# Kernel tuning notes

Hardware: AMD Instinct MI355X
Metric: run time of the kernel (lower is better)

The kernel has to match this reference:

```python
import jax, jax.numpy as jnp
import numpy as np

TEMPERATURE = 0.1
EPS = 1e-12  # tf.math.l2_normalize epsilon

BATCH = 512
DIM = 256
QUEUE = 65536


def l2_normalize(x, axis=1):
    sq = jnp.sum(x * x, axis=axis, keepdims=True)
    return x * jax.lax.rsqrt(jnp.maximum(sq, EPS))


def setup_inputs() -> dict:
    key = jax.random.key(0)
    k1, k2, k3 = jax.random.split(key, 3)
    projections_1 = jax.random.normal(k1, (BATCH, DIM), dtype=jnp.float32)
    projections_2 = jax.random.normal(k2, (BATCH, DIM), dtype=jnp.float32)
    feature_queue = l2_normalize(jax.random.normal(k3, (QUEUE, DIM), dtype=jnp.float32), axis=1)
    return {"projections_1": projections_1, "projections_2": projections_2, "feature_queue": feature_queue}


def nearest_neighbour(projections, feature_queue):
    # [B, Q] similarity vs the memory queue, 1-NN retrieval + gather
    support_similarities = jnp.einsum('bd,qd->bq', projections, feature_queue)
    nn_idx = jnp.argmax(support_similarities, axis=1)
    nn_projections = feature_queue[nn_idx]  # [B, D]
    # straight-through: forward value is nn, gradient flows to projections
    return projections + jax.lax.stop_gradient(nn_projections - projections)


def reference(projections_1, projections_2, feature_queue):
    p1 = l2_normalize(projections_1, axis=1)
    p2 = l2_normalize(projections_2, axis=1)

    nn1 = nearest_neighbour(p1, feature_queue)
    nn2 = nearest_neighbour(p2, feature_queue)

    s_1_2_1 = jnp.einsum('bd,cd->bc', nn1, p2) / TEMPERATURE
    s_1_2_2 = jnp.einsum('bd,cd->bc', p2, nn1) / TEMPERATURE
    s_2_1_1 = jnp.einsum('bd,cd->bc', nn2, p1) / TEMPERATURE
    s_2_1_2 = jnp.einsum('bd,cd->bc', p1, nn2) / TEMPERATURE

    logits = jnp.concatenate([s_1_2_1, s_1_2_2, s_2_1_1, s_2_1_2], axis=0)  # [4B, B]
    batch = p1.shape[0]
    labels = jnp.tile(jnp.arange(batch), 4)  # [4B]

    # sparse categorical crossentropy from logits
    logp = jax.nn.log_softmax(logits, axis=-1)
    loss = -logp[jnp.arange(4 * batch), labels]  # [4B]

    # FIFO queue update (normalized projections_1 pushed in front)
    new_queue = jnp.concatenate([p1, feature_queue[:-batch]], axis=0)
    return loss, new_queue
```

## Files before the change

### kernel.cpp

```cpp
#include <hip/hip_runtime.h>
#include <stdint.h>


#define BATCH  512
#define DIM    256
#define QUEUE  65536
#define MROWS  1024
#define NGRP   2048
#define MARGIN 0.01f

typedef short bf16x8 __attribute__((ext_vector_type(8)));
typedef float f32x4  __attribute__((ext_vector_type(4)));

__device__ __forceinline__ unsigned int mono_f32(float f) {
    unsigned int u = __float_as_uint(f);
    return (u & 0x80000000u) ? ~u : (u | 0x80000000u);
}
__device__ __forceinline__ float unmono_f32(unsigned int m) {
    unsigned int u = (m & 0x80000000u) ? (m ^ 0x80000000u) : ~m;
    return __uint_as_float(u);
}
__device__ __forceinline__ unsigned short f2bf(float f) {
    unsigned int u = __float_as_uint(f);
    return (unsigned short)((u + 0x7fffu + ((u >> 16) & 1u)) >> 16);
}

__global__ __launch_bounds__(256)
void k01_prep(const float* __restrict__ queue, float* __restrict__ outq,
              char* __restrict__ Qbf,
              const float* __restrict__ p1, const float* __restrict__ p2,
              float* __restrict__ Pn, float* __restrict__ PnT,
              unsigned short* __restrict__ PhiF,
              unsigned int* __restrict__ rowmaxU, unsigned long long* __restrict__ rowfinal)
{
    const int bid = blockIdx.x;
    const int t = threadIdx.x;

    if (bid < 2048) {
        const int n0 = bid * 32;
        const f32x4* qsrc = (const f32x4*)(queue + (size_t)n0 * DIM);
        f32x4* qdst = (f32x4*)(outq + (size_t)(n0 + BATCH) * DIM);
        char* tile = Qbf + (size_t)(bid >> 1) * 32768;

        f32x4 va[8];
        #pragma unroll
        for (int it = 0; it < 4; ++it) {
            const int L = it * 256 + t;
            const int r = L >> 5, c16 = L & 31;
            va[2 * it]     = qsrc[(size_t)r * 64 + c16 * 2];
            va[2 * it + 1] = qsrc[(size_t)r * 64 + c16 * 2 + 1];
        }
        #pragma unroll
        for (int it = 0; it < 4; ++it) {
            const int L = it * 256 + t;
            const int r = L >> 5, c16 = L & 31;
            f32x4 v0 = va[2 * it], v1 = va[2 * it + 1];
            if (n0 + r < QUEUE - BATCH) {
                qdst[(size_t)r * 64 + c16 * 2]     = v0;
                qdst[(size_t)r * 64 + c16 * 2 + 1] = v1;
            }
            bf16x8 bb;
            bb[0] = (short)f2bf(v0.x); bb[1] = (short)f2bf(v0.y);
            bb[2] = (short)f2bf(v0.z); bb[3] = (short)f2bf(v0.w);
            bb[4] = (short)f2bf(v1.x); bb[5] = (short)f2bf(v1.y);
            bb[6] = (short)f2bf(v1.z); bb[7] = (short)f2bf(v1.w);
            const int rr = ((bid & 1) << 5) + r;
            *(bf16x8*)(tile + rr * 512 + ((c16 ^ (rr & 31)) << 4)) = bb;
        }
    } else {
        const int sub = t >> 6, lane = t & 63;
        const int r = (bid - 2048) * 4 + sub;
        if (lane == 0) {
            rowmaxU[r] = 0u;
            rowfinal[r] = 0ull;
        }
        const float* src = (r < BATCH) ? p1 : p2;
        const int row = (r < BATCH) ? r : r - BATCH;
        float4 v = ((const float4*)(src + (size_t)row * DIM))[lane];
        float sq = v.x*v.x + v.y*v.y + v.z*v.z + v.w*v.w;
        #pragma unroll
        for (int off = 32; off; off >>= 1) sq += __shfl_xor(sq, off, 64);
        sq = fmaxf(sq, 1e-12f);
        float s = rsqrtf(sq);
        s = s * (1.5f - 0.5f * sq * s * s);
        v.x *= s; v.y *= s; v.z *= s; v.w *= s;
        ((float4*)(Pn + (size_t)r * DIM))[lane] = v;
        const int k = lane * 4;
        PnT[(size_t)(k + 0) * MROWS + r] = v.x;
        PnT[(size_t)(k + 1) * MROWS + r] = v.y;
        PnT[(size_t)(k + 2) * MROWS + r] = v.z;
        PnT[(size_t)(k + 3) * MROWS + r] = v.w;
        short4 b;
        b.x = (short)f2bf(v.x); b.y = (short)f2bf(v.y);
        b.z = (short)f2bf(v.z); b.w = (short)f2bf(v.w);
        {
            const int c = lane >> 1;
            const int idx = ((r >> 4) * 8 + (c >> 2)) * 64 + (c & 3) * 16 + (r & 15);
            *(short4*)((char*)PhiF + (size_t)idx * 16 + (lane & 1) * 8) = b;
        }
        if (r < BATCH) ((float4*)(outq + (size_t)r * DIM))[lane] = v;
    }
}

__device__ __forceinline__ void k2_stage_async(const char* __restrict__ tile,
                                               char* Bsb, int t)
{
    #pragma unroll
    for (int it = 0; it < 8; ++it) {
        const int L = it * 256 + t;
        __builtin_amdgcn_global_load_lds(
            (const __attribute__((address_space(1))) unsigned int*)(tile + (size_t)L * 16),
            (__attribute__((address_space(3))) unsigned int*)(Bsb + L * 16), 16, 0, 0);
    }
}

__global__ __launch_bounds__(256, 2)
void k2_mfma(const unsigned short* __restrict__ PhiF, const char* __restrict__ Qbf,
             float* __restrict__ cand, unsigned int* __restrict__ rowmaxU)
{
    __shared__ __align__(16) char Bs[2][32768];
    const int bid = blockIdx.x;
    const int c = (bid >> 5) * 8 + (bid & 7);
    const int s = (bid >> 3) & 3;
    const int t  = threadIdx.x;
    const int w  = t >> 6, lane = t & 63;
    const int lr = lane & 15, q = lane >> 4;
    const int mbase = s * 256 + w * 64;
    const char* chunkbase = Qbf + (size_t)(c * 4) * 32768;

    bf16x8 pfr[4][8];
    {
        const char* Pw = (const char*)PhiF;
        const int mt16b = mbase >> 4;
        #pragma unroll
        for (int mj = 0; mj < 4; ++mj)
            #pragma unroll
            for (int ks = 0; ks < 8; ++ks)
                pfr[mj][ks] = *(const bf16x8*)(Pw + ((size_t)((mt16b + mj) * 8 + ks) * 64 + lane) * 16);
    }

    k2_stage_async(chunkbase, Bs[0], t);
    __syncthreads();

    float rowmx[4] = {-1e30f, -1e30f, -1e30f, -1e30f};

    for (int tl = 0; tl < 4; ++tl) {
        if (tl < 3)
            k2_stage_async(chunkbase + (size_t)(tl + 1) * 32768, Bs[(tl + 1) & 1], t);

        char* Bsb = Bs[tl & 1];
        f32x4 acc[4][4];
        #pragma unroll
        for (int i = 0; i < 4; ++i)
            #pragma unroll
            for (int j = 0; j < 4; ++j) acc[i][j] = (f32x4){0.f, 0.f, 0.f, 0.f};

        #pragma unroll
        for (int ks = 0; ks < 8; ++ks) {
            bf16x8 qf[4];
            #pragma unroll
            for (int ni = 0; ni < 4; ++ni) {
                const int r = ni * 16 + lr;
                const int c16 = ks * 4 + q;
                qf[ni] = *(const bf16x8*)(Bsb + r * 512 + ((c16 ^ (r & 31)) << 4));
            }
            #pragma unroll
            for (int ni = 0; ni < 4; ++ni)
                #pragma unroll
                for (int mj = 0; mj < 4; ++mj)
                    acc[ni][mj] = __builtin_amdgcn_mfma_f32_16x16x32_bf16(qf[ni], pfr[mj][ks], acc[ni][mj], 0, 0, 0);
        }

        #pragma unroll
        for (int mj = 0; mj < 4; ++mj) {
            #pragma unroll
            for (int gl = 0; gl < 2; ++gl) {
                f32x4 va = acc[2 * gl][mj], vb = acc[2 * gl + 1][mj];
                float mx = fmaxf(fmaxf(fmaxf(va[0], va[1]), fmaxf(va[2], va[3])),
                                 fmaxf(fmaxf(vb[0], vb[1]), fmaxf(vb[2], vb[3])));
                mx = fmaxf(mx, __shfl_xor(mx, 16, 64));
                mx = fmaxf(mx, __shfl_xor(mx, 32, 64));
                rowmx[mj] = fmaxf(rowmx[mj], mx);
                if (q == 0)
                    cand[(size_t)(c * 8 + tl * 2 + gl) * MROWS + (mbase + mj * 16 + lr)] = mx;
            }
        }
        __syncthreads();
    }

    if (q == 0) {
        #pragma unroll
        for (int mj = 0; mj < 4; ++mj)
            atomicMax(rowmaxU + mbase + mj * 16 + lr, mono_f32(rowmx[mj]));
    }
}

__global__ __launch_bounds__(256)
void k2cd(const float* __restrict__ cand, const unsigned int* __restrict__ rowmaxU,
          const float* __restrict__ Pn, const float* __restrict__ queue,
          unsigned long long* __restrict__ rowfinal)
{
    __shared__ unsigned int hits[8192];
    __shared__ int nhits;
    const int t = threadIdx.x;
    if (t == 0) nhits = 0;
    __syncthreads();

    {
        const int ml = t & 63, gs = t >> 6;
        const int mc = blockIdx.x & 15, gc = blockIdx.x >> 4;
        const int m  = mc * 64 + ml;
        const int g0 = gc * 128 + gs * 32;
        const float thr = unmono_f32(rowmaxU[m]) - MARGIN;
        #pragma unroll 8
        for (int j = 0; j < 32; ++j) {
            if (cand[(size_t)(g0 + j) * MROWS + m] >= thr) {
                int p = atomicAdd(&nhits, 1);
                hits[p] = ((unsigned int)m << 16) | (unsigned int)(g0 + j);
            }
        }
    }
    __syncthreads();

    const int n = nhits;
    const int w = t >> 6, lane = t & 63;
    const int col_l = lane & 31, half = lane >> 5;
    for (int p = w; p < n; p += 4) {
        const unsigned int pr = hits[p];
        const int row = pr >> 16, g = pr & 0xffff;
        const int col = g * 32 + col_l;
        const float4* qp = (const float4*)(queue + (size_t)col * DIM + half * 128);
        const float4* pp = (const float4*)(Pn + (size_t)row * DIM + half * 128);
        float4 sv = {0.f, 0.f, 0.f, 0.f};
        #pragma unroll 8
        for (int j = 0; j < 32; ++j) {
            float4 a = pp[j], b = qp[j];
            sv.x = fmaf(a.x, b.x, sv.x); sv.y = fmaf(a.y, b.y, sv.y);
            sv.z = fmaf(a.z, b.z, sv.z); sv.w = fmaf(a.w, b.w, sv.w);
        }
        float s = (sv.x + sv.y) + (sv.z + sv.w);
        s += __shfl_xor(s, 32, 64);
        unsigned long long best = ((unsigned long long)mono_f32(s) << 32)
                                | (unsigned int)(65535 - col);
        #pragma unroll
        for (int off = 1; off <= 16; off <<= 1) {
            unsigned long long o = __shfl_xor(best, off, 64);
            best = best > o ? best : o;
        }
        if (lane == 0) atomicMax(rowfinal + row, best);
    }
}

__global__ void k3_sim(const unsigned long long* __restrict__ rowfinal,
                       const float* __restrict__ queue,
                       const float* __restrict__ PnT, float* __restrict__ S)
{
    const int b  = blockIdx.x;
    const int rb = (b >> 1) * 4;
    const int ch = b & 1;
    const int tid = threadIdx.x;
    const int which = (rb < BATCH) ? 0 : 1;
    const int colbase = which ? 0 : BATCH;
    const int col = colbase + ch * 256 + tid;
    __shared__ float nnv[4][DIM];
    #pragma unroll
    for (int j = 0; j < 4; ++j) {
        const int idx = 65535 - (int)(rowfinal[rb + j] & 0xFFFFull);
        nnv[j][tid] = queue[(size_t)idx * DIM + tid];
    }
    __syncthreads();
    float acc[4];
    #pragma unroll
    for (int j = 0; j < 4; ++j) acc[j] = 0.f;
    for (int k4 = 0; k4 < 64; ++k4) {
        float4 nv[4];
        #pragma unroll
        for (int j = 0; j < 4; ++j) nv[j] = ((const float4*)nnv[j])[k4];
        #pragma unroll
        for (int kk = 0; kk < 4; ++kk) {
            const int k = k4 * 4 + kk;
            const float v0 = PnT[(size_t)k * MROWS + col];
            #pragma unroll
            for (int j = 0; j < 4; ++j) {
                const float nj = ((const float*)&nv[j])[kk];
                acc[j] = fmaf(nj, v0, acc[j]);
            }
        }
    }
    const int i0 = rb & (BATCH - 1);
    float* Sout = S + (size_t)which * (BATCH * BATCH);
    #pragma unroll
    for (int j = 0; j < 4; ++j)
        Sout[(size_t)(i0 + j) * BATCH + ch * 256 + tid] = acc[j] * 10.0f;
}

__global__ void k4_loss(const float* __restrict__ S, float* __restrict__ loss)
{
    const int r = blockIdx.x;
    const int tid = threadIdx.x;
    const int grp = r >> 9;
    const int i = r & 511;
    const float* M = S + (size_t)(grp >> 1) * (BATCH * BATCH);
    float x0, x1;
    if (!(grp & 1)) { x0 = M[(size_t)i * BATCH + tid];  x1 = M[(size_t)i * BATCH + tid + 256]; }
    else            { x0 = M[(size_t)tid * BATCH + i];  x1 = M[(size_t)(tid + 256) * BATCH + i]; }
    const float diag = M[(size_t)i * BATCH + i];
    float mx = fmaxf(x0, x1);
    #pragma unroll
    for (int off = 1; off < 64; off <<= 1) mx = fmaxf(mx, __shfl_xor(mx, off, 64));
    __shared__ float redm[4], reds[4];
    if ((tid & 63) == 0) redm[tid >> 6] = mx;
    __syncthreads();
    mx = fmaxf(fmaxf(redm[0], redm[1]), fmaxf(redm[2], redm[3]));
    float e = __expf(x0 - mx) + __expf(x1 - mx);
    #pragma unroll
    for (int off = 1; off < 64; off <<= 1) e += __shfl_xor(e, off, 64);
    if ((tid & 63) == 0) reds[tid >> 6] = e;
    __syncthreads();
    if (tid == 0)
        loss[r] = mx + logf(reds[0] + reds[1] + reds[2] + reds[3]) - diag;
}

extern "C" void kernel_launch(void* const* d_in, const int* in_sizes, int n_in,
                              void* d_out, int out_size, void* d_ws, size_t ws_size,
                              hipStream_t stream)
{
    const float* p1    = (const float*)d_in[0];
    const float* p2    = (const float*)d_in[1];
    const float* queue = (const float*)d_in[2];
    float* out  = (float*)d_out;
    float* loss = out;
    float* outq = out + 4 * BATCH;

    char* w = (char*)d_ws;
    float* cand = (float*)w;                               w += (size_t)NGRP * MROWS * 4;
    unsigned long long* rowfinal = (unsigned long long*)w; w += MROWS * 8;
    unsigned int* rowmaxU = (unsigned int*)w;              w += MROWS * 4;
    float* Pn  = (float*)w;                                w += (size_t)MROWS * DIM * 4;
    float* PnT = (float*)w;                                w += (size_t)MROWS * DIM * 4;
    unsigned short* PhiF = (unsigned short*)w;             w += (size_t)MROWS * DIM * 2;
    float* S = (float*)w;                                  w += (size_t)2 * BATCH * BATCH * 4;
    char* Qbf = w;

    hipLaunchKernelGGL(k01_prep,    dim3(2048 + 256), dim3(256), 0, stream,
                       queue, outq, Qbf, p1, p2, Pn, PnT, PhiF, rowmaxU, rowfinal);
    hipLaunchKernelGGL(k2_mfma,     dim3(1024), dim3(256), 0, stream, PhiF, Qbf, cand, rowmaxU);
    hipLaunchKernelGGL(k2cd,        dim3(256),  dim3(256), 0, stream, cand, rowmaxU, Pn, queue, rowfinal);
    hipLaunchKernelGGL(k3_sim,      dim3(512),  dim3(256), 0, stream, rowfinal, queue, PnT, S);
    hipLaunchKernelGGL(k4_loss,     dim3(4 * BATCH), dim3(256), 0, stream, S, loss);
}
```

Baseline: 213.7 us.

## Deepen k2 LDS pipeline to four half-tile buffers with explicit vmcnt waits

The MFMA similarity kernel now stages the queue tile in 16 KB halves across a four-deep LDS ring, prefetching two halves ahead. It uses explicit s_waitcnt vmcnt counts and raw s_barrier in place of __syncthreads, so async loads can stay in flight across iterations. The prep kernel is also reordered so the small normalization blocks launch first, letting the dependent data get produced early. The risk is a correctness hazard if the hand-counted vmcnt values are wrong, and there are more barriers per unit of work.

```diff
diff --git a/kernel.cpp b/kernel.cpp
--- a/kernel.cpp
+++ b/kernel.cpp
@@ -36,11 +36,12 @@
     const int bid = blockIdx.x;
     const int t = threadIdx.x;
 
-    if (bid < 2048) {
-        const int n0 = bid * 32;
+    if (bid >= 256) {
+        const int b0 = bid - 256;
+        const int n0 = b0 * 32;
         const f32x4* qsrc = (const f32x4*)(queue + (size_t)n0 * DIM);
         f32x4* qdst = (f32x4*)(outq + (size_t)(n0 + BATCH) * DIM);
-        char* tile = Qbf + (size_t)(bid >> 1) * 32768;
+        char* tile = Qbf + (size_t)(b0 >> 1) * 32768;
 
         f32x4 va[8];
         #pragma unroll
@@ -64,12 +65,12 @@
             bb[2] = (short)f2bf(v0.z); bb[3] = (short)f2bf(v0.w);
             bb[4] = (short)f2bf(v1.x); bb[5] = (short)f2bf(v1.y);
             bb[6] = (short)f2bf(v1.z); bb[7] = (short)f2bf(v1.w);
-            const int rr = ((bid & 1) << 5) + r;
+            const int rr = ((b0 & 1) << 5) + r;
             *(bf16x8*)(tile + rr * 512 + ((c16 ^ (rr & 31)) << 4)) = bb;
         }
     } else {
         const int sub = t >> 6, lane = t & 63;
-        const int r = (bid - 2048) * 4 + sub;
+        const int r = bid * 4 + sub;
         if (lane == 0) {
             rowmaxU[r] = 0u;
             rowfinal[r] = 0ull;
@@ -102,15 +103,15 @@
     }
 }
 
-__device__ __forceinline__ void k2_stage_async(const char* __restrict__ tile,
-                                               char* Bsb, int t)
-{
-    #pragma unroll
-    for (int it = 0; it < 8; ++it) {
+__device__ __forceinline__ void k2_stage_half(const char* __restrict__ src,
+                                              char* dst, int t)
+{
+    #pragma unroll
+    for (int it = 0; it < 4; ++it) {
         const int L = it * 256 + t;
         __builtin_amdgcn_global_load_lds(
-            (const __attribute__((address_space(1))) unsigned int*)(tile + (size_t)L * 16),
-            (__attribute__((address_space(3))) unsigned int*)(Bsb + L * 16), 16, 0, 0);
+            (const __attribute__((address_space(1))) unsigned int*)(src + (size_t)L * 16),
+            (__attribute__((address_space(3))) unsigned int*)(dst + L * 16), 16, 0, 0);
     }
 }
 
@@ -118,7 +119,7 @@
 void k2_mfma(const unsigned short* __restrict__ PhiF, const char* __restrict__ Qbf,
              float* __restrict__ cand, unsigned int* __restrict__ rowmaxU)
 {
-    __shared__ __align__(16) char Bs[2][32768];
+    __shared__ __align__(16) char Bs[4][16384];
     const int bid = blockIdx.x;
     const int c = (bid >> 5) * 8 + (bid & 7);
     const int s = (bid >> 3) & 3;
@@ -139,33 +140,41 @@
                 pfr[mj][ks] = *(const bf16x8*)(Pw + ((size_t)((mt16b + mj) * 8 + ks) * 64 + lane) * 16);
     }
 
-    k2_stage_async(chunkbase, Bs[0], t);
-    __syncthreads();
+    k2_stage_half(chunkbase,         Bs[0], t);
+    k2_stage_half(chunkbase + 16384, Bs[1], t);
 
     float rowmx[4] = {-1e30f, -1e30f, -1e30f, -1e30f};
 
-    for (int tl = 0; tl < 4; ++tl) {
-        if (tl < 3)
-            k2_stage_async(chunkbase + (size_t)(tl + 1) * 32768, Bs[(tl + 1) & 1], t);
-
-        char* Bsb = Bs[tl & 1];
-        f32x4 acc[4][4];
-        #pragma unroll
-        for (int i = 0; i < 4; ++i)
+    #pragma unroll
+    for (int h = 0; h < 8; ++h) {
+        if (h + 2 < 8)
+            k2_stage_half(chunkbase + (size_t)(h + 2) * 16384, Bs[(h + 2) & 3], t);
+
+        if (h == 0)      asm volatile("s_waitcnt vmcnt(8)"  ::: "memory");
+        else if (h <= 5) asm volatile("s_waitcnt vmcnt(12)" ::: "memory");
+        else if (h == 6) asm volatile("s_waitcnt vmcnt(8)"  ::: "memory");
+        else             asm volatile("s_waitcnt vmcnt(4)"  ::: "memory");
+        __builtin_amdgcn_s_barrier();
+        __builtin_amdgcn_sched_barrier(0);
+
+        const char* Bsb = Bs[h & 3];
+        f32x4 acc[2][4];
+        #pragma unroll
+        for (int i = 0; i < 2; ++i)
             #pragma unroll
             for (int j = 0; j < 4; ++j) acc[i][j] = (f32x4){0.f, 0.f, 0.f, 0.f};
 
         #pragma unroll
         for (int ks = 0; ks < 8; ++ks) {
-            bf16x8 qf[4];
-            #pragma unroll
-            for (int ni = 0; ni < 4; ++ni) {
-                const int r = ni * 16 + lr;
+            bf16x8 qf[2];
+            #pragma unroll
+            for (int ni = 0; ni < 2; ++ni) {
+                const int rl = ni * 16 + lr;
                 const int c16 = ks * 4 + q;
-                qf[ni] = *(const bf16x8*)(Bsb + r * 512 + ((c16 ^ (r & 31)) << 4));
+                qf[ni] = *(const bf16x8*)(Bsb + rl * 512 + ((c16 ^ rl) << 4));
             }
             #pragma unroll
-            for (int ni = 0; ni < 4; ++ni)
+            for (int ni = 0; ni < 2; ++ni)
                 #pragma unroll
                 for (int mj = 0; mj < 4; ++mj)
                     acc[ni][mj] = __builtin_amdgcn_mfma_f32_16x16x32_bf16(qf[ni], pfr[mj][ks], acc[ni][mj], 0, 0, 0);
@@ -173,19 +182,17 @@
 
         #pragma unroll
         for (int mj = 0; mj < 4; ++mj) {
-            #pragma unroll
-            for (int gl = 0; gl < 2; ++gl) {
-                f32x4 va = acc[2 * gl][mj], vb = acc[2 * gl + 1][mj];
-                float mx = fmaxf(fmaxf(fmaxf(va[0], va[1]), fmaxf(va[2], va[3])),
-                                 fmaxf(fmaxf(vb[0], vb[1]), fmaxf(vb[2], vb[3])));
-                mx = fmaxf(mx, __shfl_xor(mx, 16, 64));
-                mx = fmaxf(mx, __shfl_xor(mx, 32, 64));
-                rowmx[mj] = fmaxf(rowmx[mj], mx);
-                if (q == 0)
-                    cand[(size_t)(c * 8 + tl * 2 + gl) * MROWS + (mbase + mj * 16 + lr)] = mx;
-            }
-        }
-        __syncthreads();
+            f32x4 va = acc[0][mj], vb = acc[1][mj];
+            float mx = fmaxf(fmaxf(fmaxf(va[0], va[1]), fmaxf(va[2], va[3])),
+                             fmaxf(fmaxf(vb[0], vb[1]), fmaxf(vb[2], vb[3])));
+            mx = fmaxf(mx, __shfl_xor(mx, 16, 64));
+            mx = fmaxf(mx, __shfl_xor(mx, 32, 64));
+            rowmx[mj] = fmaxf(rowmx[mj], mx);
+            if (q == 0)
+                cand[(size_t)(c * 8 + h) * MROWS + (mbase + mj * 16 + lr)] = mx;
+        }
+        __builtin_amdgcn_s_barrier();
+        __builtin_amdgcn_sched_barrier(0);
     }
 
     if (q == 0) {
@@ -342,7 +349,7 @@
     float* S = (float*)w;                                  w += (size_t)2 * BATCH * BATCH * 4;
     char* Qbf = w;
 
-    hipLaunchKernelGGL(k01_prep,    dim3(2048 + 256), dim3(256), 0, stream,
+    hipLaunchKernelGGL(k01_prep,    dim3(256 + 2048), dim3(256), 0, stream,
                        queue, outq, Qbf, p1, p2, Pn, PnT, PhiF, rowmaxU, rowfinal);
     hipLaunchKernelGGL(k2_mfma,     dim3(1024), dim3(256), 0, stream, PhiF, Qbf, cand, rowmaxU);
     hipLaunchKernelGGL(k2cd,        dim3(256),  dim3(256), 0, stream, cand, rowmaxU, Pn, queue, rowfinal);
```

Result: no change. 213.4 us (-0.1%).
